# Optimization experiments

Hardware: AMD Instinct MI355X
Metric: run time of the kernel (lower is better)

The kernel has to match this reference:

```python
import jax, jax.numpy as jnp
import numpy as np

BS, Z_DIM, HID, Z_IN, N_STEP, OUT_DIM = 4096, 512, 1024, 128, 32, 3


def setup_inputs() -> dict:
    key = jax.random.key(0)
    ks = jax.random.split(key, 12)
    s = 0.02
    return {
        "z": jax.random.normal(ks[0], (BS, Z_DIM), jnp.float32),
        "inference": 1,
        "tfr": 0,
        "W_zh": jax.random.normal(ks[1], (HID, Z_DIM), jnp.float32) * s,
        "b_zh": jnp.zeros((HID,), jnp.float32),
        "W_zi": jax.random.normal(ks[2], (Z_IN, Z_DIM), jnp.float32) * s,
        "b_zi": jnp.zeros((Z_IN,), jnp.float32),
        "W_ih": jax.random.normal(ks[3], (3 * HID, OUT_DIM + Z_IN), jnp.float32) * s,
        "b_ih": jnp.zeros((3 * HID,), jnp.float32),
        "W_hh": jax.random.normal(ks[4], (3 * HID, HID), jnp.float32) * s,
        "b_hh": jnp.zeros((3 * HID,), jnp.float32),
        "W_out": jax.random.normal(ks[5], (OUT_DIM, HID), jnp.float32) * s,
        "b_out": jnp.zeros((OUT_DIM,), jnp.float32),
        "init_input": jax.random.uniform(ks[6], (OUT_DIM,), jnp.float32),
    }


def reference(z, inference, tfr, W_zh, b_zh, W_zi, b_zi, W_ih, b_ih, W_hh, b_hh,
              W_out, b_out, init_input):
    bs = z.shape[0]
    h0 = z @ W_zh.T + b_zh                      # [B, H]   (z2dec_hid)
    z_in = z @ W_zi.T + b_zi                    # [B, Z_IN] (z2dec_in)
    token0 = jnp.broadcast_to(init_input, (bs, OUT_DIM))

    def step(carry, _):
        h, token = carry
        x = jnp.concatenate([token, z_in], axis=-1)     # [B, OUT_DIM+Z_IN]
        gi = x @ W_ih.T + b_ih                          # [B, 3H]
        gh = h @ W_hh.T + b_hh                          # [B, 3H]
        i_r, i_u, i_n = jnp.split(gi, 3, axis=-1)       # pytorch gate order r,z,n
        h_r, h_u, h_n = jnp.split(gh, 3, axis=-1)
        r = jax.nn.sigmoid(i_r + h_r)
        u = jax.nn.sigmoid(i_u + h_u)
        n = jnp.tanh(i_n + r * h_n)
        h_new = (1.0 - u) * n + u * h
        o = h_new @ W_out.T + b_out                     # [B, 3]
        bass = jax.nn.sigmoid(o[:, 0])
        rhy_int = o[:, 1]
        rhy = jax.nn.sigmoid(o[:, 2])
        out_feat = jnp.stack([bass, rhy_int, rhy], axis=-1)          # [B, 3]
        next_token = jnp.stack(
            [bass, rhy_int, (rhy > 0.5).astype(z.dtype)], axis=-1)  # [B, 3]
        return (h_new, next_token), out_feat

    _, outs = jax.lax.scan(step, (h0, token0), None, length=N_STEP)  # [T, B, 3]
    recon = jnp.transpose(outs, (1, 0, 2))                           # [B, T, 3]
    return recon
```

## Files before the change

kernel.cpp:

```cpp
#include <hip/hip_runtime.h>
#include <hip/hip_bf16.h>
#include <math.h>

#define BS   4096
#define ZD   512
#define HIDN 1024
#define ZINN 128
#define NST  32
#define NP   3072

typedef unsigned short u16;
typedef __bf16 bf16x8 __attribute__((ext_vector_type(8)));
typedef _Float16 f16x8 __attribute__((ext_vector_type(8)));
typedef float f32x4 __attribute__((ext_vector_type(4)));
typedef float f32x16 __attribute__((ext_vector_type(16)));

static __device__ __forceinline__ u16 bf_bits(float v) {
  __bf16 b = (__bf16)v;
  return __builtin_bit_cast(unsigned short, b);
}
static __device__ __forceinline__ float bf_val(float v) {
  return (float)(__bf16)v;
}
static __device__ __forceinline__ u16 h16_bits(float v) {
  _Float16 h = (_Float16)v;
  return __builtin_bit_cast(unsigned short, h);
}

static __device__ __forceinline__ void ld_lds16(const u16* g, u16* l) {
  __builtin_amdgcn_global_load_lds(
      (const __attribute__((address_space(1))) void*)g,
      (__attribute__((address_space(3))) void*)l, 16, 0, 0);
}

static __device__ __forceinline__ int r_orig(int w) {
  const int g = w / 96;
  const int rem = w - g * 96;
  const int j = rem >> 5, m = rem & 31;
  return j * 1024 + g * 32 + m;
}

static __device__ __forceinline__ size_t pk_off(int row, int col) {
  return ((size_t)(row >> 5) * 64 + (col >> 4)) * 512 +
         (((col >> 3) & 1) * 32 + (row & 31)) * 8 + (col & 7);
}
static __device__ __forceinline__ size_t pkz_off(int row, int col) {
  return ((size_t)(row >> 5) * 8 + (col >> 4)) * 512 +
         (((col >> 3) & 1) * 32 + (row & 31)) * 8 + (col & 7);
}


__global__ void k_split(const float* __restrict__ s, u16* __restrict__ hi,
                        u16* __restrict__ lo, int n) {
  int i = blockIdx.x * 256 + threadIdx.x;
  if (i >= n) return;
  float v = s[i];
  float h = bf_val(v);
  hi[i] = bf_bits(v);
  lo[i] = bf_bits(v - h);
}

__global__ void k_pack_whh(const float* __restrict__ W_hh, u16* __restrict__ Bpk) {
  int i = blockIdx.x * 256 + threadIdx.x;
  if (i >= NP * HIDN) return;
  const int w = i >> 10, k = i & 1023;
  const float v = W_hh[(size_t)r_orig(w) * HIDN + k];
  Bpk[pk_off(w, k)] = h16_bits(v);
}

__global__ void k_prep_wih(const float* __restrict__ W_ih, const float* __restrict__ b_ih,
                           const float* __restrict__ b_hh,
                           u16* __restrict__ Wpk,
                           float* __restrict__ wtok, float* __restrict__ cb0) {
  int i = blockIdx.x * 256 + threadIdx.x;
  if (i < NP * 128) {
    const int w = i >> 7, c = i & 127;
    const float v = W_ih[r_orig(w) * 131 + 3 + c];
    Wpk[pkz_off(w, c)] = h16_bits(v);
  }
  if (i < NP * 3) {
    const int w = i / 3, s = i - w * 3;
    wtok[i] = W_ih[r_orig(w) * 131 + s];
  }
  if (i < NP) {
    const int r = r_orig(i);
    cb0[i] = b_ih[r] + (r < 2048 ? b_hh[r] : 0.0f);
  }
}

__global__ void k_token_init(const float* __restrict__ init_input, float* __restrict__ token) {
  int i = blockIdx.x * 256 + threadIdx.x;
  if (i < BS * 4) token[i] = ((i & 3) < 3) ? init_input[i & 3] : 0.0f;
}

template <int OUTMODE>
__global__ __launch_bounds__(256) void k_gemm(
    const u16* __restrict__ Ahi, const u16* __restrict__ Alo,
    const u16* __restrict__ Bhi, const u16* __restrict__ Blo,
    const float* __restrict__ bias,
    float* __restrict__ C, u16* __restrict__ Apk, int N, int K) {
  __shared__ __align__(16) u16 sAhi[128 * 64];
  __shared__ __align__(16) u16 sAlo[128 * 64];
  __shared__ __align__(16) u16 sBhi[128 * 64];
  __shared__ __align__(16) u16 sBlo[128 * 64];

  const int t = threadIdx.x;
  const int row0 = blockIdx.y * 128, col0 = blockIdx.x * 128;
  const int wave = t >> 6, lane = t & 63;
  const int w64 = wave * 64;
  const int wm = (wave & 1) * 64, wn = (wave >> 1) * 64;
  const int lm = lane & 15, lq = lane >> 4;
  const int pb = lm & 7;

  f32x4 acc[4][4] = {};

  int sm[4], skc[4], sub[4];
#pragma unroll
  for (int i = 0; i < 4; ++i) {
    const int u = i * 256 + t;
    sm[i] = u >> 3;
    skc[i] = (u & 7) ^ (sm[i] & 7);
    sub[i] = (i * 256 + w64) * 8;
  }

  const int nk = K >> 6;
  for (int kt = 0; kt < nk; ++kt) {
    const int k0 = kt << 6;
    __syncthreads();
#pragma unroll
    for (int i = 0; i < 4; ++i) {
      const size_t ga = (size_t)(row0 + sm[i]) * K + k0 + skc[i] * 8;
      const size_t gb = (size_t)(col0 + sm[i]) * K + k0 + skc[i] * 8;
      ld_lds16(Ahi + ga, &sAhi[sub[i]]);
      ld_lds16(Alo + ga, &sAlo[sub[i]]);
      ld_lds16(Bhi + gb, &sBhi[sub[i]]);
      ld_lds16(Blo + gb, &sBlo[sub[i]]);
    }
    __syncthreads();
#pragma unroll
    for (int kk = 0; kk < 2; ++kk) {
      const int pos = ((kk * 4 + lq) ^ pb) * 8;
      bf16x8 ah[4], al[4], bh[4], bl[4];
#pragma unroll
      for (int i = 0; i < 4; ++i) {
        const int ma = (wm + i * 16 + lm) * 64;
        const int mb = (wn + i * 16 + lm) * 64;
        ah[i] = *(const bf16x8*)&sAhi[ma + pos];
        al[i] = *(const bf16x8*)&sAlo[ma + pos];
        bh[i] = *(const bf16x8*)&sBhi[mb + pos];
        bl[i] = *(const bf16x8*)&sBlo[mb + pos];
      }
#pragma unroll
      for (int i = 0; i < 4; ++i)
#pragma unroll
        for (int j = 0; j < 4; ++j) {
          acc[i][j] = __builtin_amdgcn_mfma_f32_16x16x32_bf16(ah[i], bh[j], acc[i][j], 0, 0, 0);
          acc[i][j] = __builtin_amdgcn_mfma_f32_16x16x32_bf16(al[i], bh[j], acc[i][j], 0, 0, 0);
          acc[i][j] = __builtin_amdgcn_mfma_f32_16x16x32_bf16(ah[i], bl[j], acc[i][j], 0, 0, 0);
        }
    }
  }

#pragma unroll
  for (int i = 0; i < 4; ++i) {
    const int grow = row0 + wm + i * 16 + lq * 4;
#pragma unroll
    for (int j = 0; j < 4; ++j) {
      const int gcol = col0 + wn + j * 16 + lm;
      const float bs = bias ? bias[gcol] : 0.0f;
#pragma unroll
      for (int d = 0; d < 4; ++d) {
        const float v = acc[i][j][d] + bs;
        if (OUTMODE == 2) {
          C[(size_t)(grow + d) * N + gcol] = v;
          Apk[pk_off(grow + d, gcol)] = h16_bits(v);
        }
        if (OUTMODE == 3) {
          Apk[pkz_off(grow + d, gcol)] = h16_bits(v);
        }
      }
    }
  }
}


#define SZA8 (128 * 64)
#define SZB8 (192 * 64)
#define MF8(a, b, c) c = __builtin_amdgcn_mfma_f32_32x32x16_f16(a, b, c, 0, 0, 0)

__global__ __launch_bounds__(512, 4) void k_fused12(
    const u16* __restrict__ Apk,
    const u16* __restrict__ Bpk,
    const u16* __restrict__ Zpk,
    const u16* __restrict__ Wpk,
    const float* __restrict__ token,
    const float* __restrict__ wtok,
    const float* __restrict__ cb0,
    const float* __restrict__ b_hh,
    const float* __restrict__ h_in, float* __restrict__ h_out,
    u16* __restrict__ Apk_out) {
  __shared__ __align__(16) u16 sA[2 * SZA8];
  __shared__ __align__(16) u16 sB[2 * SZB8];

  const int t = threadIdx.x;
  const int wave = t >> 6, lane = t & 63;
  const int row0 = blockIdx.y * 128;
  const int colW0 = blockIdx.x * 192;
  const int wm = (wave >> 1) * 32;
  const int wn = (wave & 1) * 96;
  const int lr = lane & 31, lh = lane >> 5;

  f32x16 acc0 = {}, acc1 = {}, acc2 = {}, acc3 = {};

  const u16* asrc = Apk + ((size_t)((row0 >> 5) + (wave >> 1)) * 64 + (wave & 1) * 2) * 512 + lane * 8;
  const int aw = (wave >> 1) * 2048 + (wave & 1) * 1024;
  const int id0 = wave * 3, id1 = id0 + 1, id2 = id0 + 2;
  const u16* bsrc0 = Bpk + ((size_t)((colW0 >> 5) + (id0 >> 2)) * 64 + (id0 & 3)) * 512 + lane * 8;
  const u16* bsrc1 = Bpk + ((size_t)((colW0 >> 5) + (id1 >> 2)) * 64 + (id1 & 3)) * 512 + lane * 8;
  const u16* bsrc2 = Bpk + ((size_t)((colW0 >> 5) + (id2 >> 2)) * 64 + (id2 & 3)) * 512 + lane * 8;
  const int bw0 = id0 * 512, bw1 = id1 * 512, bw2 = id2 * 512;
  const u16* azb = Zpk + ((size_t)((row0 >> 5) + (wave >> 1)) * 8 + (wave & 1) * 2) * 512 + lane * 8;
  const u16* bzb0 = Wpk + ((size_t)((colW0 >> 5) + (id0 >> 2)) * 8 + (id0 & 3)) * 512 + lane * 8;
  const u16* bzb1 = Wpk + ((size_t)((colW0 >> 5) + (id1 >> 2)) * 8 + (id1 & 3)) * 512 + lane * 8;
  const u16* bzb2 = Wpk + ((size_t)((colW0 >> 5) + (id2 >> 2)) * 8 + (id2 & 3)) * 512 + lane * 8;

#define STAGE(kt_, ab, bb)                                            \
  ld_lds16(asrc + (size_t)(kt_) * 2048,       &sA[(ab) + aw]);        \
  ld_lds16(asrc + (size_t)(kt_) * 2048 + 512, &sA[(ab) + aw + 512]);  \
  ld_lds16(bsrc0 + (size_t)(kt_) * 2048, &sB[(bb) + bw0]);            \
  ld_lds16(bsrc1 + (size_t)(kt_) * 2048, &sB[(bb) + bw1]);            \
  ld_lds16(bsrc2 + (size_t)(kt_) * 2048, &sB[(bb) + bw2]);

#define STAGE_Z(zt_, ab, bb)                                          \
  ld_lds16(azb + (zt_) * 2048,       &sA[(ab) + aw]);                 \
  ld_lds16(azb + (zt_) * 2048 + 512, &sA[(ab) + aw + 512]);           \
  ld_lds16(bzb0 + (zt_) * 2048, &sB[(bb) + bw0]);                     \
  ld_lds16(bzb1 + (zt_) * 2048, &sB[(bb) + bw1]);                     \
  ld_lds16(bzb2 + (zt_) * 2048, &sB[(bb) + bw2]);

  const int agA = (wave >> 1) * 2048;
  const int bgB = (wave & 1) * 6144;
  const int l8 = lane * 8;

  STAGE(0, 0, 0);
  __syncthreads();

#pragma unroll 1
  for (int kt = 0; kt < 16; ++kt) {
    const int ab = (kt & 1) ? SZA8 : 0, bb = (kt & 1) ? SZB8 : 0;
    const int an = (kt & 1) ? 0 : SZA8, bn = (kt & 1) ? 0 : SZB8;
    if (kt < 15) { STAGE(kt + 1, an, bn); }
    else         { STAGE_Z(0, an, bn); }
#pragma unroll
    for (int kk = 0; kk < 4; ++kk) {
      const f16x8 a = *(const f16x8*)&sA[ab + agA + kk * 512 + l8];
      const int kb = bb + bgB + kk * 512 + l8;
      const f16x8 b0 = *(const f16x8*)&sB[kb];
      const f16x8 b1 = *(const f16x8*)&sB[kb + 2048];
      const f16x8 b2 = *(const f16x8*)&sB[kb + 4096];
      MF8(a, b0, acc0); MF8(a, b1, acc1); MF8(a, b2, acc2);
    }
    __syncthreads();
  }
  STAGE_Z(1, SZA8, SZB8);
#pragma unroll
  for (int kk = 0; kk < 4; ++kk) {
    const f16x8 a = *(const f16x8*)&sA[agA + kk * 512 + l8];
    const int kb = bgB + kk * 512 + l8;
    const f16x8 b0 = *(const f16x8*)&sB[kb];
    const f16x8 b1 = *(const f16x8*)&sB[kb + 2048];
    const f16x8 b2 = *(const f16x8*)&sB[kb + 4096];
    MF8(a, b0, acc0); MF8(a, b1, acc1); MF8(a, b2, acc3);
  }
  __syncthreads();
#pragma unroll
  for (int kk = 0; kk < 4; ++kk) {
    const f16x8 a = *(const f16x8*)&sA[SZA8 + agA + kk * 512 + l8];
    const int kb = SZB8 + bgB + kk * 512 + l8;
    const f16x8 b0 = *(const f16x8*)&sB[kb];
    const f16x8 b1 = *(const f16x8*)&sB[kb + 2048];
    const f16x8 b2 = *(const f16x8*)&sB[kb + 4096];
    MF8(a, b0, acc0); MF8(a, b1, acc1); MF8(a, b2, acc3);
  }
#undef STAGE
#undef STAGE_Z

  const int w0 = colW0 + wn + lr;
  const int c = ((colW0 + wn) / 96) * 32 + lr;
  float wt[3][3];
#pragma unroll
  for (int j = 0; j < 3; ++j) {
    wt[j][0] = wtok[(w0 + j * 32) * 3 + 0];
    wt[j][1] = wtok[(w0 + j * 32) * 3 + 1];
    wt[j][2] = wtok[(w0 + j * 32) * 3 + 2];
  }
  const float cbr = cb0[w0], cbu = cb0[w0 + 32], cbn = cb0[w0 + 64];
  const float bnn = b_hh[2048 + c];
  const int cq = c >> 4, ckh = (c >> 3) & 1, ce = c & 7;
#pragma unroll
  for (int d = 0; d < 16; ++d) {
    const int row = row0 + wm + 4 * lh + (d & 3) + 8 * (d >> 2);
    const float4 tk = *(const float4*)&token[row * 4];
    const float pr = cbr + acc0[d] + tk.x * wt[0][0] + tk.y * wt[0][1] + tk.z * wt[0][2];
    const float pu = cbu + acc1[d] + tk.x * wt[1][0] + tk.y * wt[1][1] + tk.z * wt[1][2];
    const float pin = cbn + acc3[d] + tk.x * wt[2][0] + tk.y * wt[2][1] + tk.z * wt[2][2];
    const float hn = acc2[d] + bnn;
    const float r = 1.0f / (1.0f + expf(-pr));
    const float u = 1.0f / (1.0f + expf(-pu));
    const float n = tanhf(pin + r * hn);
    const size_t hidx = (size_t)row * HIDN + c;
    const float hv = (1.0f - u) * n + u * h_in[hidx];
    h_out[hidx] = hv;
    const size_t poff = ((size_t)(row >> 5) * 64 + cq) * 512 + (ckh * 32 + (row & 31)) * 8 + ce;
    Apk_out[poff] = h16_bits(hv);
  }
}
#undef MF8

__global__ __launch_bounds__(256) void k_out(
    const u16* __restrict__ Apk, const float* __restrict__ W_out,
    const float* __restrict__ b_out,
    float* __restrict__ out, float* __restrict__ token, int step) {
  const int wave = threadIdx.x >> 6, lane = threadIdx.x & 63;
  const int row = blockIdx.x * 4 + wave;
  const u16* base = Apk + (size_t)(row >> 5) * 64 * 512 + (row & 31) * 8;
  float s0 = 0.f, s1 = 0.f, s2 = 0.f;
#pragma unroll
  for (int cc = 0; cc < 2; ++cc) {
    const int ch = lane + cc * 64;
    const f16x8 hv = *(const f16x8*)&base[(ch >> 1) * 512 + (ch & 1) * 256];
    const int k0 = ch * 8;
#pragma unroll
    for (int e = 0; e < 8; ++e) {
      const float hf = (float)hv[e];
      s0 += hf * W_out[k0 + e];
      s1 += hf * W_out[1024 + k0 + e];
      s2 += hf * W_out[2048 + k0 + e];
    }
  }
#pragma unroll
  for (int off = 32; off > 0; off >>= 1) {
    s0 += __shfl_xor(s0, off, 64);
    s1 += __shfl_xor(s1, off, 64);
    s2 += __shfl_xor(s2, off, 64);
  }
  if (lane == 0) {
    const float o0 = s0 + b_out[0];
    const float o1 = s1 + b_out[1];
    const float o2 = s2 + b_out[2];
    const float bass = 1.0f / (1.0f + expf(-o0));
    const float rhy = 1.0f / (1.0f + expf(-o2));
    const size_t ob = ((size_t)row * NST + step) * 3;
    out[ob + 0] = bass;
    out[ob + 1] = o1;
    out[ob + 2] = rhy;
    token[row * 4 + 0] = bass;
    token[row * 4 + 1] = o1;
    token[row * 4 + 2] = (rhy > 0.5f) ? 1.0f : 0.0f;
  }
}

extern "C" void kernel_launch(void* const* d_in, const int* in_sizes, int n_in,
                              void* d_out, int out_size, void* d_ws, size_t ws_size,
                              hipStream_t stream) {
  const float* z = (const float*)d_in[0];
  const float* W_zh = (const float*)d_in[3];
  const float* b_zh = (const float*)d_in[4];
  const float* W_zi = (const float*)d_in[5];
  const float* b_zi = (const float*)d_in[6];
  const float* W_ih = (const float*)d_in[7];
  const float* b_ih = (const float*)d_in[8];
  const float* W_hh = (const float*)d_in[9];
  const float* b_hh = (const float*)d_in[10];
  const float* W_out = (const float*)d_in[11];
  const float* b_out = (const float*)d_in[12];
  const float* init_input = (const float*)d_in[13];
  float* out = (float*)d_out;

  char* p = (char*)d_ws;
  auto alloc = [&](size_t bytes) {
    char* q = p;
    p += (bytes + 255) & ~(size_t)255;
    return q;
  };
  float* h[2];
  u16* Apk[2];
  for (int s = 0; s < 2; ++s) {
    h[s] = (float*)alloc((size_t)BS * HIDN * 4);
    Apk[s] = (u16*)alloc((size_t)BS * 1024 * 2);
  }
  u16* Bpk = (u16*)alloc((size_t)NP * 1024 * 2);
  u16* Zpk = (u16*)alloc((size_t)BS * 128 * 2);
  u16* Wpk = (u16*)alloc((size_t)NP * 128 * 2);
  u16* z_hi = (u16*)alloc((size_t)BS * ZD * 2);
  u16* z_lo = (u16*)alloc((size_t)BS * ZD * 2);
  u16* Wzh_hi = (u16*)alloc((size_t)HIDN * ZD * 2);
  u16* Wzh_lo = (u16*)alloc((size_t)HIDN * ZD * 2);
  u16* Wzi_hi = (u16*)alloc((size_t)ZINN * ZD * 2);
  u16* Wzi_lo = (u16*)alloc((size_t)ZINN * ZD * 2);
  float* wtok = (float*)alloc((size_t)NP * 3 * 4);
  float* cb0 = (float*)alloc((size_t)NP * 4);
  float* token = (float*)alloc((size_t)BS * 4 * 4);

  k_pack_whh<<<dim3((NP * HIDN + 255) / 256), 256, 0, stream>>>(W_hh, Bpk);
  k_split<<<dim3((HIDN * ZD + 255) / 256), 256, 0, stream>>>(W_zh, Wzh_hi, Wzh_lo, HIDN * ZD);
  k_split<<<dim3((ZINN * ZD + 255) / 256), 256, 0, stream>>>(W_zi, Wzi_hi, Wzi_lo, ZINN * ZD);
  k_split<<<dim3((BS * ZD + 255) / 256), 256, 0, stream>>>(z, z_hi, z_lo, BS * ZD);
  k_prep_wih<<<dim3((NP * 128 + 255) / 256), 256, 0, stream>>>(W_ih, b_ih, b_hh, Wpk, wtok, cb0);
  k_token_init<<<dim3((BS * 4 + 255) / 256), 256, 0, stream>>>(init_input, token);

  k_gemm<2><<<dim3(HIDN / 128, BS / 128), 256, 0, stream>>>(
      z_hi, z_lo, Wzh_hi, Wzh_lo, b_zh, h[0], Apk[0], HIDN, ZD);
  k_gemm<3><<<dim3(ZINN / 128, BS / 128), 256, 0, stream>>>(
      z_hi, z_lo, Wzi_hi, Wzi_lo, b_zi, nullptr, Zpk, ZINN, ZD);

  for (int t = 0; t < NST; ++t) {
    const int cur = t & 1, nxt = (t + 1) & 1;
    k_fused12<<<dim3(NP / 192, BS / 128), 512, 0, stream>>>(
        Apk[cur], Bpk, Zpk, Wpk, token, wtok, cb0, b_hh,
        h[cur], h[nxt], Apk[nxt]);
    k_out<<<dim3(BS / 4), 256, 0, stream>>>(Apk[nxt], W_out, b_out, out, token, t);
  }
  (void)in_sizes; (void)n_in; (void)out_size; (void)ws_size;
}
```

Measured before the change: 1.697 ms.

## Use 4 waves with 64x96 warp tiles and warp-specialized loads in fused GRU step

The fused GRU step kernel drops from 8 waves to 4 per block, and each wave now computes a 64x96 output tile (2x3 MFMA 32x32 tiles) instead of 32x96. Each A and B fragment read from LDS now feeds more MFMAs, cutting LDS reads per flop. Global-to-LDS staging is also specialized: two waves load the A tile and two load the B tile, replacing the even split across all waves. Accumulator registers per wave double, which may lower occupancy, and the loads are no longer balanced across waves.

```diff
diff --git a/kernel.cpp b/kernel.cpp
--- a/kernel.cpp
+++ b/kernel.cpp
@@ -184,11 +184,11 @@
 }
 
 
-#define SZA8 (128 * 64)
-#define SZB8 (192 * 64)
-#define MF8(a, b, c) c = __builtin_amdgcn_mfma_f32_32x32x16_f16(a, b, c, 0, 0, 0)
-
-__global__ __launch_bounds__(512, 4) void k_fused12(
+#define SZA13 8192
+#define SZB13 12288
+#define MF13(a, b, c) c = __builtin_amdgcn_mfma_f32_32x32x16_f16(a, b, c, 0, 0, 0)
+
+__global__ __launch_bounds__(256, 2) void k_fused13(
     const u16* __restrict__ Apk,
     const u16* __restrict__ Bpk,
     const u16* __restrict__ Zpk,
@@ -199,90 +199,109 @@
     const float* __restrict__ b_hh,
     const float* __restrict__ h_in, float* __restrict__ h_out,
     u16* __restrict__ Apk_out) {
-  __shared__ __align__(16) u16 sA[2 * SZA8];
-  __shared__ __align__(16) u16 sB[2 * SZB8];
+  __shared__ __align__(16) u16 sA[2 * SZA13];
+  __shared__ __align__(16) u16 sB[2 * SZB13];
 
   const int t = threadIdx.x;
   const int wave = t >> 6, lane = t & 63;
   const int row0 = blockIdx.y * 128;
   const int colW0 = blockIdx.x * 192;
-  const int wm = (wave >> 1) * 32;
+  const int wm = (wave >> 1) * 64;
   const int wn = (wave & 1) * 96;
   const int lr = lane & 31, lh = lane >> 5;
-
-  f32x16 acc0 = {}, acc1 = {}, acc2 = {}, acc3 = {};
-
-  const u16* asrc = Apk + ((size_t)((row0 >> 5) + (wave >> 1)) * 64 + (wave & 1) * 2) * 512 + lane * 8;
-  const int aw = (wave >> 1) * 2048 + (wave & 1) * 1024;
-  const int id0 = wave * 3, id1 = id0 + 1, id2 = id0 + 2;
-  const u16* bsrc0 = Bpk + ((size_t)((colW0 >> 5) + (id0 >> 2)) * 64 + (id0 & 3)) * 512 + lane * 8;
-  const u16* bsrc1 = Bpk + ((size_t)((colW0 >> 5) + (id1 >> 2)) * 64 + (id1 & 3)) * 512 + lane * 8;
-  const u16* bsrc2 = Bpk + ((size_t)((colW0 >> 5) + (id2 >> 2)) * 64 + (id2 & 3)) * 512 + lane * 8;
-  const int bw0 = id0 * 512, bw1 = id1 * 512, bw2 = id2 * 512;
-  const u16* azb = Zpk + ((size_t)((row0 >> 5) + (wave >> 1)) * 8 + (wave & 1) * 2) * 512 + lane * 8;
-  const u16* bzb0 = Wpk + ((size_t)((colW0 >> 5) + (id0 >> 2)) * 8 + (id0 & 3)) * 512 + lane * 8;
-  const u16* bzb1 = Wpk + ((size_t)((colW0 >> 5) + (id1 >> 2)) * 8 + (id1 & 3)) * 512 + lane * 8;
-  const u16* bzb2 = Wpk + ((size_t)((colW0 >> 5) + (id2 >> 2)) * 8 + (id2 & 3)) * 512 + lane * 8;
-
-#define STAGE(kt_, ab, bb)                                            \
-  ld_lds16(asrc + (size_t)(kt_) * 2048,       &sA[(ab) + aw]);        \
-  ld_lds16(asrc + (size_t)(kt_) * 2048 + 512, &sA[(ab) + aw + 512]);  \
-  ld_lds16(bsrc0 + (size_t)(kt_) * 2048, &sB[(bb) + bw0]);            \
-  ld_lds16(bsrc1 + (size_t)(kt_) * 2048, &sB[(bb) + bw1]);            \
-  ld_lds16(bsrc2 + (size_t)(kt_) * 2048, &sB[(bb) + bw2]);
-
-#define STAGE_Z(zt_, ab, bb)                                          \
-  ld_lds16(azb + (zt_) * 2048,       &sA[(ab) + aw]);                 \
-  ld_lds16(azb + (zt_) * 2048 + 512, &sA[(ab) + aw + 512]);           \
-  ld_lds16(bzb0 + (zt_) * 2048, &sB[(bb) + bw0]);                     \
-  ld_lds16(bzb1 + (zt_) * 2048, &sB[(bb) + bw1]);                     \
-  ld_lds16(bzb2 + (zt_) * 2048, &sB[(bb) + bw2]);
-
-  const int agA = (wave >> 1) * 2048;
+  const int l8 = lane * 8;
+
+  f32x16 acc[2][4] = {};
+
+  const bool isAw = (wave < 2);
+  const u16* gH;
+  const u16* gZ;
+  int ldsb;
+  if (isAw) {
+    gH = Apk + ((size_t)((row0 >> 5) + wave * 2) * 64) * 512 + l8;
+    gZ = Zpk + ((size_t)((row0 >> 5) + wave * 2) * 8) * 512 + l8;
+    ldsb = wave * 4096;
+  } else {
+    gH = Bpk + ((size_t)((colW0 >> 5) + (wave - 2) * 3) * 64) * 512 + l8;
+    gZ = Wpk + ((size_t)((colW0 >> 5) + (wave - 2) * 3) * 8) * 512 + l8;
+    ldsb = (wave - 2) * 6144;
+  }
+
+#define STAGE_H(kt_, ab, bb)                                                      \
+  if (isAw) {                                                                     \
+    _Pragma("unroll") for (int i = 0; i < 8; ++i)                                 \
+      ld_lds16(gH + (size_t)(kt_) * 2048 + (i >> 2) * 32768 + (i & 3) * 512,      \
+               &sA[(ab) + ldsb + i * 512]);                                       \
+  } else {                                                                        \
+    _Pragma("unroll") for (int i = 0; i < 12; ++i)                                \
+      ld_lds16(gH + (size_t)(kt_) * 2048 + (i >> 2) * 32768 + (i & 3) * 512,      \
+               &sB[(bb) + ldsb + i * 512]);                                       \
+  }
+
+#define STAGE_Z(zt_, ab, bb)                                                      \
+  if (isAw) {                                                                     \
+    _Pragma("unroll") for (int i = 0; i < 8; ++i)                                 \
+      ld_lds16(gZ + (size_t)(zt_) * 2048 + (i >> 2) * 4096 + (i & 3) * 512,       \
+               &sA[(ab) + ldsb + i * 512]);                                       \
+  } else {                                                                        \
+    _Pragma("unroll") for (int i = 0; i < 12; ++i)                                \
+      ld_lds16(gZ + (size_t)(zt_) * 2048 + (i >> 2) * 4096 + (i & 3) * 512,       \
+               &sB[(bb) + ldsb + i * 512]);                                       \
+  }
+
+  const int agA = (wave >> 1) * 4096;
   const int bgB = (wave & 1) * 6144;
-  const int l8 = lane * 8;
-
-  STAGE(0, 0, 0);
+
+  STAGE_H(0, 0, 0);
   __syncthreads();
 
 #pragma unroll 1
   for (int kt = 0; kt < 16; ++kt) {
-    const int ab = (kt & 1) ? SZA8 : 0, bb = (kt & 1) ? SZB8 : 0;
-    const int an = (kt & 1) ? 0 : SZA8, bn = (kt & 1) ? 0 : SZB8;
-    if (kt < 15) { STAGE(kt + 1, an, bn); }
+    const int ab = (kt & 1) ? SZA13 : 0, bb = (kt & 1) ? SZB13 : 0;
+    const int an = (kt & 1) ? 0 : SZA13, bn = (kt & 1) ? 0 : SZB13;
+    if (kt < 15) { STAGE_H(kt + 1, an, bn); }
     else         { STAGE_Z(0, an, bn); }
 #pragma unroll
     for (int kk = 0; kk < 4; ++kk) {
-      const f16x8 a = *(const f16x8*)&sA[ab + agA + kk * 512 + l8];
+      const f16x8 a0 = *(const f16x8*)&sA[ab + agA + kk * 512 + l8];
+      const f16x8 a1 = *(const f16x8*)&sA[ab + agA + 2048 + kk * 512 + l8];
       const int kb = bb + bgB + kk * 512 + l8;
       const f16x8 b0 = *(const f16x8*)&sB[kb];
       const f16x8 b1 = *(const f16x8*)&sB[kb + 2048];
       const f16x8 b2 = *(const f16x8*)&sB[kb + 4096];
-      MF8(a, b0, acc0); MF8(a, b1, acc1); MF8(a, b2, acc2);
+      MF13(a0, b0, acc[0][0]); MF13(a1, b0, acc[1][0]);
+      MF13(a0, b1, acc[0][1]); MF13(a1, b1, acc[1][1]);
+      MF13(a0, b2, acc[0][2]); MF13(a1, b2, acc[1][2]);
     }
     __syncthreads();
   }
-  STAGE_Z(1, SZA8, SZB8);
+  STAGE_Z(1, SZA13, SZB13);
 #pragma unroll
   for (int kk = 0; kk < 4; ++kk) {
-    const f16x8 a = *(const f16x8*)&sA[agA + kk * 512 + l8];
+    const f16x8 a0 = *(const f16x8*)&sA[agA + kk * 512 + l8];
+    const f16x8 a1 = *(const f16x8*)&sA[agA + 2048 + kk * 512 + l8];
     const int kb = bgB + kk * 512 + l8;
     const f16x8 b0 = *(const f16x8*)&sB[kb];
     const f16x8 b1 = *(const f16x8*)&sB[kb + 2048];
     const f16x8 b2 = *(const f16x8*)&sB[kb + 4096];
-    MF8(a, b0, acc0); MF8(a, b1, acc1); MF8(a, b2, acc3);
+    MF13(a0, b0, acc[0][0]); MF13(a1, b0, acc[1][0]);
+    MF13(a0, b1, acc[0][1]); MF13(a1, b1, acc[1][1]);
+    MF13(a0, b2, acc[0][3]); MF13(a1, b2, acc[1][3]);
   }
   __syncthreads();
 #pragma unroll
   for (int kk = 0; kk < 4; ++kk) {
-    const f16x8 a = *(const f16x8*)&sA[SZA8 + agA + kk * 512 + l8];
-    const int kb = SZB8 + bgB + kk * 512 + l8;
+    const f16x8 a0 = *(const f16x8*)&sA[SZA13 + agA + kk * 512 + l8];
+    const f16x8 a1 = *(const f16x8*)&sA[SZA13 + agA + 2048 + kk * 512 + l8];
+    const int kb = SZB13 + bgB + kk * 512 + l8;
     const f16x8 b0 = *(const f16x8*)&sB[kb];
     const f16x8 b1 = *(const f16x8*)&sB[kb + 2048];
     const f16x8 b2 = *(const f16x8*)&sB[kb + 4096];
-    MF8(a, b0, acc0); MF8(a, b1, acc1); MF8(a, b2, acc3);
-  }
-#undef STAGE
+    MF13(a0, b0, acc[0][0]); MF13(a1, b0, acc[1][0]);
+    MF13(a0, b1, acc[0][1]); MF13(a1, b1, acc[1][1]);
+    MF13(a0, b2, acc[0][3]); MF13(a1, b2, acc[1][3]);
+  }
+#undef STAGE_H
 #undef STAGE_Z
 
   const int w0 = colW0 + wn + lr;
@@ -298,24 +317,27 @@
   const float bnn = b_hh[2048 + c];
   const int cq = c >> 4, ckh = (c >> 3) & 1, ce = c & 7;
 #pragma unroll
-  for (int d = 0; d < 16; ++d) {
-    const int row = row0 + wm + 4 * lh + (d & 3) + 8 * (d >> 2);
-    const float4 tk = *(const float4*)&token[row * 4];
-    const float pr = cbr + acc0[d] + tk.x * wt[0][0] + tk.y * wt[0][1] + tk.z * wt[0][2];
-    const float pu = cbu + acc1[d] + tk.x * wt[1][0] + tk.y * wt[1][1] + tk.z * wt[1][2];
-    const float pin = cbn + acc3[d] + tk.x * wt[2][0] + tk.y * wt[2][1] + tk.z * wt[2][2];
-    const float hn = acc2[d] + bnn;
-    const float r = 1.0f / (1.0f + expf(-pr));
-    const float u = 1.0f / (1.0f + expf(-pu));
-    const float n = tanhf(pin + r * hn);
-    const size_t hidx = (size_t)row * HIDN + c;
-    const float hv = (1.0f - u) * n + u * h_in[hidx];
-    h_out[hidx] = hv;
-    const size_t poff = ((size_t)(row >> 5) * 64 + cq) * 512 + (ckh * 32 + (row & 31)) * 8 + ce;
-    Apk_out[poff] = h16_bits(hv);
-  }
-}
-#undef MF8
+  for (int mi = 0; mi < 2; ++mi) {
+#pragma unroll
+    for (int d = 0; d < 16; ++d) {
+      const int row = row0 + wm + mi * 32 + 4 * lh + (d & 3) + 8 * (d >> 2);
+      const float4 tk = *(const float4*)&token[row * 4];
+      const float pr = cbr + acc[mi][0][d] + tk.x * wt[0][0] + tk.y * wt[0][1] + tk.z * wt[0][2];
+      const float pu = cbu + acc[mi][1][d] + tk.x * wt[1][0] + tk.y * wt[1][1] + tk.z * wt[1][2];
+      const float pin = cbn + acc[mi][3][d] + tk.x * wt[2][0] + tk.y * wt[2][1] + tk.z * wt[2][2];
+      const float hn = acc[mi][2][d] + bnn;
+      const float r = 1.0f / (1.0f + expf(-pr));
+      const float u = 1.0f / (1.0f + expf(-pu));
+      const float n = tanhf(pin + r * hn);
+      const size_t hidx = (size_t)row * HIDN + c;
+      const float hv = (1.0f - u) * n + u * h_in[hidx];
+      h_out[hidx] = hv;
+      const size_t poff = ((size_t)(row >> 5) * 64 + cq) * 512 + (ckh * 32 + (row & 31)) * 8 + ce;
+      Apk_out[poff] = h16_bits(hv);
+    }
+  }
+}
+#undef MF13
 
 __global__ __launch_bounds__(256) void k_out(
     const u16* __restrict__ Apk, const float* __restrict__ W_out,
@@ -416,7 +438,7 @@
 
   for (int t = 0; t < NST; ++t) {
     const int cur = t & 1, nxt = (t + 1) & 1;
-    k_fused12<<<dim3(NP / 192, BS / 128), 512, 0, stream>>>(
+    k_fused13<<<dim3(NP / 192, BS / 128), 256, 0, stream>>>(
         Apk[cur], Bpk, Zpk, Wpk, token, wtok, cb0, b_hh,
         h[cur], h[nxt], Apk[nxt]);
     k_out<<<dim3(BS / 4), 256, 0, stream>>>(Apk[nxt], W_out, b_out, out, token, t);
```

New measurement: 1.784 ms. +5.2%, slower.
